# Performance work log

Measured on AMD Instinct MI355X. Metric: run time of the kernel, lower is better.

## Reference

```python
import jax, jax.numpy as jnp
import numpy as np

DIM = 768
H = 12          # num query heads
KV = 6          # num kv heads
GS = H // KV    # group size = 2
HD = DIM // H   # head dim = 64


def setup_inputs() -> dict:
    key = jax.random.key(0)
    ks = jax.random.split(key, 6)
    B, P = 8, 1024
    s = DIM ** -0.5
    x = jax.random.normal(ks[0], (B, P, DIM), dtype=jnp.float32)
    Wq = jax.random.normal(ks[1], (DIM, DIM), dtype=jnp.float32) * s
    Wk = jax.random.normal(ks[2], (DIM, KV * HD), dtype=jnp.float32) * s
    Wv = jax.random.normal(ks[3], (DIM, KV * HD), dtype=jnp.float32) * s
    Wp = jax.random.normal(ks[4], (DIM, DIM), dtype=jnp.float32) * s
    bp = jnp.zeros((DIM,), dtype=jnp.float32)
    return {"x": x, "Wq": Wq, "Wk": Wk, "Wv": Wv, "Wp": Wp, "bp": bp}


def reference(x, Wq, Wk, Wv, Wp, bp):
    B, P, C = x.shape
    scale = HD ** -0.5
    # projections; consecutive heads i*GS..(i+1)*GS-1 form kv-group i (torch.split dim=1)
    q = (x @ Wq).reshape(B, P, KV, GS, HD).transpose(0, 2, 3, 1, 4) * scale  # [B,KV,GS,P,d]
    k = (x @ Wk).reshape(B, P, KV, HD).transpose(0, 2, 1, 3)                 # [B,KV,P,d]
    v = (x @ Wv).reshape(B, P, KV, HD).transpose(0, 2, 1, 3)                 # [B,KV,P,d]

    scores = jnp.einsum('bghqd,bgkd->bghqk', q, k)      # [B,KV,GS,P,P]
    w = jax.nn.softmax(scores, axis=-1)                  # attn_drop=0 (eval)
    att = jnp.einsum('bghqk,bgkd->bghqd', w, v)          # [B,KV,GS,P,d]

    # per-group row-matched gaussian-ish noise (torch get_gaussian), vectorized over KV groups
    y = P * HD
    flat = att.reshape(B, KV, GS, y)                     # rows = groups within kv-group
    M = jax.random.uniform(jax.random.key(42), (KV, GS, y), dtype=flat.dtype)
    di = jnp.arange(min(GS, y))
    M = M.at[:, di, di].set(0.0)                         # sparse: zero diagonal
    m_mean = M.mean(axis=-1, keepdims=True)
    m_std = jnp.std(M, axis=-1, ddof=1, keepdims=True)   # torch.std is unbiased
    m_std = jnp.where(m_std == 0, jnp.ones_like(m_std), m_std)
    Z = (M - m_mean) / m_std                             # [KV,GS,y], shared across batch
    r_mean = flat.mean(axis=-1, keepdims=True)           # [B,KV,GS,1]
    r_std = jnp.std(flat, axis=-1, ddof=1, keepdims=True)
    flat = flat - (Z[None] * r_std + r_mean)

    att = flat.reshape(B, KV, GS, P, HD).reshape(B, H, P, HD)
    out = att.transpose(0, 2, 1, 3).reshape(B, P, C) @ Wp + bp  # proj_drop=0
    return out
```

## Files before the change

kernel.cpp:

```cpp
#include <hip/hip_runtime.h>
#include <hip/hip_bf16.h>
#include <math.h>


#define NTHREADS 256

typedef __bf16 bf16x8 __attribute__((ext_vector_type(8)));
typedef float f32x4 __attribute__((ext_vector_type(4)));

#define MFMA16(a, b, c) __builtin_amdgcn_mfma_f32_16x16x32_bf16(a, b, c, 0, 0, 0)

#define QSCALE 0.18033688011112042f

__device__ __forceinline__ float fexp2(float x) {
#if __has_builtin(__builtin_amdgcn_exp2f)
    return __builtin_amdgcn_exp2f(x);
#else
    return __expf(x * 0.6931471805599453f);
#endif
}

__device__ __forceinline__ void gload16(const void* g, void* l) {
    __builtin_amdgcn_global_load_lds(
        (const __attribute__((address_space(1))) void*)g,
        (__attribute__((address_space(3))) void*)l, 16, 0, 0);
}

__device__ __forceinline__ unsigned rotl_u32(unsigned x, int r) {
    return (x << r) | (x >> (32 - r));
}
__device__ __forceinline__ void threefry_0_42(unsigned x0, unsigned x1,
                                              unsigned& o0, unsigned& o1) {
    const unsigned ks0 = 0u, ks1 = 42u, ks2 = 0u ^ 42u ^ 0x1BD11BDAu;
    x0 += ks0; x1 += ks1;
#define R4(a,b,c,d) \
    x0 += x1; x1 = rotl_u32(x1,a); x1 ^= x0; \
    x0 += x1; x1 = rotl_u32(x1,b); x1 ^= x0; \
    x0 += x1; x1 = rotl_u32(x1,c); x1 ^= x0; \
    x0 += x1; x1 = rotl_u32(x1,d); x1 ^= x0;
    R4(13,15,26,6)   x0 += ks1; x1 += ks2 + 1u;
    R4(17,29,16,24)  x0 += ks2; x1 += ks0 + 2u;
    R4(13,15,26,6)   x0 += ks0; x1 += ks1 + 3u;
    R4(17,29,16,24)  x0 += ks1; x1 += ks2 + 4u;
    R4(13,15,26,6)   x0 += ks2; x1 += ks0 + 5u;
#undef R4
    o0 = x0; o1 = x1;
}
__device__ __forceinline__ float tf_uniform(unsigned i) {
    unsigned o0, o1;
    threefry_0_42(0u, i, o0, o1);
    unsigned bits = o0 ^ o1;
    return __uint_as_float((bits >> 9) | 0x3f800000u) - 1.0f;
}

__device__ __forceinline__ float wave_sum64(float v) {
#pragma unroll
    for (int off = 32; off; off >>= 1) v += __shfl_xor(v, off, 64);
    return v;
}

__device__ __forceinline__ unsigned short bf16_rne(float x) {
    unsigned u = __float_as_uint(x);
    return (unsigned short)((u + 0x7fffu + ((u >> 16) & 1u)) >> 16);
}
__device__ __forceinline__ unsigned pack_bf16x2(float lo, float hi) {
    return (unsigned)bf16_rne(lo) | ((unsigned)bf16_rne(hi) << 16);
}
__device__ __forceinline__ float bfu(unsigned v) {
    return __uint_as_float(v << 16);
}

__global__ __launch_bounds__(NTHREADS) void prep_k(
    const float* __restrict__ x, const float* __restrict__ Wq,
    const float* __restrict__ Wk, const float* __restrict__ Wv,
    const float* __restrict__ Wp,
    unsigned short* __restrict__ xb, unsigned short* __restrict__ wqt,
    unsigned short* __restrict__ wkt, unsigned short* __restrict__ wvt,
    unsigned short* __restrict__ wpt,
    unsigned short* __restrict__ zb, float* __restrict__ zpart)
{
    __shared__ float rbuf[8];
    int blk = blockIdx.x;
    if (blk < 1536) {
#pragma unroll
        for (int j = 0; j < 4; ++j) {
            int i = blk * 1024 + j * 256 + threadIdx.x;
            float4 v = ((const float4*)x)[i];
            uint2 u;
            u.x = pack_bf16x2(v.x, v.y);
            u.y = pack_bf16x2(v.z, v.w);
            *(uint2*)(xb + (size_t)i * 4) = u;
        }
    } else if (blk < 1920) {
        int zc = blk - 1536;
        int row = zc >> 5, chunk = zc & 31;
        int g = row & 1;
        int j0 = chunk * 2048;
        float sum = 0.f, sumsq = 0.f;
        for (int t = threadIdx.x; t < 2048; t += NTHREADS) {
            int j = j0 + t;
            unsigned i = (unsigned)row * 65536u + (unsigned)j;
            float m = tf_uniform(i);
            if (j == g) m = 0.f;
            zb[i] = bf16_rne(m);
            sum += m; sumsq += m * m;
        }
        sum = wave_sum64(sum); sumsq = wave_sum64(sumsq);
        int lane = threadIdx.x & 63, wv = threadIdx.x >> 6;
        if (lane == 0) { rbuf[wv] = sum; rbuf[4 + wv] = sumsq; }
        __syncthreads();
        if (threadIdx.x == 0) {
            zpart[zc * 2]     = rbuf[0] + rbuf[1] + rbuf[2] + rbuf[3];
            zpart[zc * 2 + 1] = rbuf[4] + rbuf[5] + rbuf[6] + rbuf[7];
        }
    } else {
        int id = blk - 1920;
        const float* W; unsigned short* Wt; int N;
        if (id < 144)      { W = Wq; Wt = wqt; N = 768; }
        else if (id < 216) { W = Wk; Wt = wkt; N = 384; id -= 144; }
        else if (id < 288) { W = Wv; Wt = wvt; N = 384; id -= 216; }
        else               { W = Wp; Wt = wpt; N = 768; id -= 288; }
        int ntn = N >> 6;
        int kt = id / ntn, nt = id % ntn;
        int k0 = kt * 64, n0 = nt * 64;
        int t = threadIdx.x;
        int tn = t & 63, tk = t >> 6;
        float r[16];
#pragma unroll
        for (int j = 0; j < 16; ++j)
            r[j] = W[(size_t)(k0 + tk * 16 + j) * N + n0 + tn];
        uint4 u0, u1;
        u0.x = pack_bf16x2(r[0], r[1]);   u0.y = pack_bf16x2(r[2], r[3]);
        u0.z = pack_bf16x2(r[4], r[5]);   u0.w = pack_bf16x2(r[6], r[7]);
        u1.x = pack_bf16x2(r[8], r[9]);   u1.y = pack_bf16x2(r[10], r[11]);
        u1.z = pack_bf16x2(r[12], r[13]); u1.w = pack_bf16x2(r[14], r[15]);
        unsigned short* dst = Wt + (size_t)(n0 + tn) * 768 + k0 + tk * 16;
        *(uint4*)dst = u0;
        *(uint4*)(dst + 8) = u1;
    }
}

__device__ __forceinline__ void mfma_tile_compute(
    const unsigned short* __restrict__ A, const unsigned short* __restrict__ Bt,
    int row0, int col0,
    unsigned short* As, unsigned short* Bs, f32x4 acc[4][4])
{
    const int tid = threadIdx.x;
    const int w = tid >> 6, lane = tid & 63;
    const int c = lane & 15, g = lane >> 4;
    const int m0 = (w & 1) * 64, n0 = (w >> 1) * 64;

#pragma unroll
    for (int mi = 0; mi < 4; ++mi)
#pragma unroll
        for (int ni = 0; ni < 4; ++ni) acc[mi][ni] = (f32x4){0.f, 0.f, 0.f, 0.f};

    const unsigned short* Ag0 = A + (size_t)(row0 + w * 16 + c) * 768 + g * 8;
    const unsigned short* Ag1 = A + (size_t)(row0 + (w + 4) * 16 + c) * 768 + g * 8;
    const unsigned short* Bg0 = Bt + (size_t)(col0 + w * 16 + c) * 768 + g * 8;
    const unsigned short* Bg1 = Bt + (size_t)(col0 + (w + 4) * 16 + c) * 768 + g * 8;
    unsigned short* Al0 = As + w * 1024 + lane * 8;
    unsigned short* Al1 = As + (w + 4) * 1024 + lane * 8;
    unsigned short* Bl0 = Bs + w * 1024 + lane * 8;
    unsigned short* Bl1 = Bs + (w + 4) * 1024 + lane * 8;

    for (int k0 = 0; k0 < 768; k0 += 64) {
        __syncthreads();
        gload16(Ag0 + k0,      Al0);
        gload16(Ag0 + k0 + 32, Al0 + 512);
        gload16(Ag1 + k0,      Al1);
        gload16(Ag1 + k0 + 32, Al1 + 512);
        gload16(Bg0 + k0,      Bl0);
        gload16(Bg0 + k0 + 32, Bl0 + 512);
        gload16(Bg1 + k0,      Bl1);
        gload16(Bg1 + k0 + 32, Bl1 + 512);
        __syncthreads();
#pragma unroll
        for (int ks = 0; ks < 2; ++ks) {
            bf16x8 aA[4], bB[4];
#pragma unroll
            for (int mi = 0; mi < 4; ++mi)
                aA[mi] = *(const bf16x8*)&As[(size_t)((m0 >> 4) + mi) * 1024 + ks * 512 + g * 128 + c * 8];
#pragma unroll
            for (int ni = 0; ni < 4; ++ni)
                bB[ni] = *(const bf16x8*)&Bs[(size_t)((n0 >> 4) + ni) * 1024 + ks * 512 + g * 128 + c * 8];
#pragma unroll
            for (int mi = 0; mi < 4; ++mi)
#pragma unroll
                for (int ni = 0; ni < 4; ++ni)
                    acc[mi][ni] = MFMA16(aA[mi], bB[ni], acc[mi][ni]);
        }
    }
}

__global__ __launch_bounds__(NTHREADS) void qkv_mfma_k(
    const unsigned short* __restrict__ xb, const unsigned short* __restrict__ wqt,
    const unsigned short* __restrict__ wkt, const unsigned short* __restrict__ wvt,
    unsigned short* __restrict__ qbh, unsigned short* __restrict__ kb2,
    unsigned short* __restrict__ vb2)
{
    __shared__ unsigned short As[8192];
    __shared__ unsigned short Bs[8192];
    int id = blockIdx.x;
    int xcd = id & 7, slot = id >> 3;
    int y0i = xcd + ((slot & 7) << 3);
    int nb  = slot >> 3;
    int y0 = y0i * 128;
    f32x4 acc[4][4];

    const int tid = threadIdx.x;
    const int w = tid >> 6, lane = tid & 63;
    const int c = lane & 15, g = lane >> 4;
    const int m0 = (w & 1) * 64, n0 = (w >> 1) * 64;

    if (nb < 9) {
        int row0 = (nb < 6) ? nb * 128 : (nb - 6) * 128;
        const unsigned short* Wt = (nb < 6) ? wqt : wkt;
        mfma_tile_compute(Wt, xb, row0, y0, As, Bs, acc);
        float scale = (nb < 6) ? QSCALE : 1.0f;
#pragma unroll
        for (int mi = 0; mi < 4; ++mi) {
            int ocol = row0 + m0 + mi * 16 + g * 4;
#pragma unroll
            for (int ni = 0; ni < 4; ++ni) {
                int pglob = y0 + n0 + ni * 16 + c;
                int b = pglob >> 10, pin = pglob & 1023;
                ushort4 u;
                u.x = bf16_rne(acc[mi][ni][0] * scale);
                u.y = bf16_rne(acc[mi][ni][1] * scale);
                u.z = bf16_rne(acc[mi][ni][2] * scale);
                u.w = bf16_rne(acc[mi][ni][3] * scale);
                if (nb < 6) {
                    int h = ocol >> 6, d0 = ocol & 63;
                    *(ushort4*)&qbh[(((size_t)b * 12 + h) * 1024 + pin) * 64 + d0] = u;
                } else {
                    int kv = ocol >> 6, d0 = ocol & 63;
                    int kt = pin >> 7, key = pin & 127;
                    *(ushort4*)&kb2[((((size_t)(b * 6 + kv) * 8 + kt) * 8 + (d0 >> 3)) * 128
                                     + key) * 8 + (d0 & 7)] = u;
                }
            }
        }
    } else {
        int col0 = (nb - 9) * 128;
        mfma_tile_compute(xb, wvt, y0, col0, As, Bs, acc);
#pragma unroll
        for (int mi = 0; mi < 4; ++mi) {
            int pglob = y0 + m0 + mi * 16 + g * 4;
            int b = pglob >> 10, pin = pglob & 1023;
            int kt = pin >> 7, pg = (pin & 127) >> 3, p8 = pin & 7;
#pragma unroll
            for (int ni = 0; ni < 4; ++ni) {
                int vcol = col0 + n0 + ni * 16 + c;
                int kv = vcol >> 6, d = vcol & 63;
                ushort4 u;
                u.x = bf16_rne(acc[mi][ni][0]);
                u.y = bf16_rne(acc[mi][ni][1]);
                u.z = bf16_rne(acc[mi][ni][2]);
                u.w = bf16_rne(acc[mi][ni][3]);
                *(ushort4*)&vb2[((((size_t)(b * 6 + kv) * 8 + kt) * 16 + pg) * 64 + d) * 8 + p8] = u;
            }
        }
    }
}

__global__ __launch_bounds__(NTHREADS) void proj_mfma_k(
    const unsigned short* __restrict__ attb, const unsigned short* __restrict__ wpt,
    const float* __restrict__ bp, float* __restrict__ out)
{
    __shared__ unsigned short As[8192];
    __shared__ unsigned short Bs[8192];
    int id = blockIdx.x;
    int xcd = id & 7, slot = id >> 3;
    int col0i = xcd + ((slot & 7) << 3);
    int row0i = slot >> 3;
    int row0 = row0i * 128, col0 = col0i * 128;
    f32x4 acc[4][4];
    mfma_tile_compute(wpt, attb, row0, col0, As, Bs, acc);

    const int tid = threadIdx.x;
    const int w = tid >> 6, lane = tid & 63;
    const int c = lane & 15, g = lane >> 4;
    const int m0 = (w & 1) * 64, n0 = (w >> 1) * 64;
#pragma unroll
    for (int mi = 0; mi < 4; ++mi) {
        int ocol = row0 + m0 + mi * 16 + g * 4;
        float4 bias = *(const float4*)&bp[ocol];
#pragma unroll
        for (int ni = 0; ni < 4; ++ni) {
            int p = col0 + n0 + ni * 16 + c;
            float4 u;
            u.x = acc[mi][ni][0] + bias.x;
            u.y = acc[mi][ni][1] + bias.y;
            u.z = acc[mi][ni][2] + bias.z;
            u.w = acc[mi][ni][3] + bias.w;
            *(float4*)&out[(size_t)p * 768 + ocol] = u;
        }
    }
}

#define LDP 136
__global__ __launch_bounds__(NTHREADS) void attn_mfma_k(
    const unsigned short* __restrict__ qbh, const unsigned short* __restrict__ kb2,
    const unsigned short* __restrict__ vb2, unsigned short* __restrict__ attb,
    float* __restrict__ spart)
{
    __shared__ unsigned short P_lds[4 * 32 * LDP];
    __shared__ float l_s[4][32];
    __shared__ float sbuf[8];

    int id = blockIdx.x;
    int xcd = id & 7, slot = id >> 3;
    int grp = slot % 6, member = slot / 6;
    int g48 = xcd + 8 * grp;
    int b = g48 / 6, kv = g48 % 6;
    int h = kv * 2 + (member & 1);
    int qtile = member >> 1;
    const int qt0 = qtile * 128;

    const int tid = threadIdx.x;
    const int w = tid >> 6, lane = tid & 63;
    const int c = lane & 15, g = lane >> 4;

    const unsigned short* qh = qbh + (((size_t)b * 12 + h) * 1024 + qt0 + w * 32) * 64;
    const unsigned short* kbase = kb2 + ((size_t)(b * 6 + kv) * 8) * 8192;
    const unsigned short* vbase = vb2 + ((size_t)(b * 6 + kv) * 8) * 8192;
    unsigned short* Pw = P_lds + w * 32 * LDP;

    bf16x8 bQ[2][2];
#pragma unroll
    for (int ks = 0; ks < 2; ++ks) {
        bQ[ks][0] = *(const bf16x8*)(qh + (size_t)(c) * 64 + ks * 32 + g * 8);
        bQ[ks][1] = *(const bf16x8*)(qh + (size_t)(16 + c) * 64 + ks * 32 + g * 8);
    }

    f32x4 O[2][4];
#pragma unroll
    for (int i = 0; i < 2; ++i)
#pragma unroll
        for (int j = 0; j < 4; ++j) O[i][j] = (f32x4){0.f, 0.f, 0.f, 0.f};
    float l_r[2] = {0.f, 0.f};

    for (int t = 0; t < 8; ++t) {
        const unsigned short* kt = kbase + (size_t)t * 8192;
        const unsigned short* vt = vbase + (size_t)t * 8192;

        bf16x8 aK[2][8];
#pragma unroll
        for (int ks = 0; ks < 2; ++ks)
#pragma unroll
            for (int mb = 0; mb < 8; ++mb)
                aK[ks][mb] = *(const bf16x8*)(kt + ((size_t)(ks * 4 + g) * 128 + mb * 16 + c) * 8);

        f32x4 S[8][2];
#pragma unroll
        for (int mb = 0; mb < 8; ++mb) {
            S[mb][0] = (f32x4){0.f, 0.f, 0.f, 0.f};
            S[mb][1] = (f32x4){0.f, 0.f, 0.f, 0.f};
        }
#pragma unroll
        for (int ks = 0; ks < 2; ++ks)
#pragma unroll
            for (int mb = 0; mb < 8; ++mb) {
                S[mb][0] = MFMA16(aK[ks][mb], bQ[ks][0], S[mb][0]);
                S[mb][1] = MFMA16(aK[ks][mb], bQ[ks][1], S[mb][1]);
            }

        bf16x8 bV[4][4];
#pragma unroll
        for (int ks = 0; ks < 4; ++ks)
#pragma unroll
            for (int nb = 0; nb < 4; ++nb)
                bV[ks][nb] = *(const bf16x8*)(vt + ((size_t)(ks * 4 + g) * 64 + nb * 16 + c) * 8);

#pragma unroll
        for (int qn = 0; qn < 2; ++qn) {
            float lt = 0.f;
#pragma unroll
            for (int mb = 0; mb < 8; ++mb) {
                float p0 = fexp2(S[mb][qn][0]);
                float p1 = fexp2(S[mb][qn][1]);
                float p2 = fexp2(S[mb][qn][2]);
                float p3 = fexp2(S[mb][qn][3]);
                lt += (p0 + p1) + (p2 + p3);
                uint2 uu;
                uu.x = pack_bf16x2(p0, p1);
                uu.y = pack_bf16x2(p2, p3);
                *(uint2*)&Pw[(size_t)(qn * 16 + c) * LDP + mb * 16 + g * 4] = uu;
            }
            lt += __shfl_xor(lt, 16, 64);
            lt += __shfl_xor(lt, 32, 64);
            l_r[qn] += lt;
        }

#pragma unroll
        for (int ks = 0; ks < 4; ++ks) {
            bf16x8 aP0 = *(const bf16x8*)&Pw[(size_t)(c) * LDP + ks * 32 + g * 8];
            bf16x8 aP1 = *(const bf16x8*)&Pw[(size_t)(16 + c) * LDP + ks * 32 + g * 8];
#pragma unroll
            for (int nb = 0; nb < 4; ++nb) {
                O[0][nb] = MFMA16(aP0, bV[ks][nb], O[0][nb]);
                O[1][nb] = MFMA16(aP1, bV[ks][nb], O[1][nb]);
            }
        }
    }
    if (g == 0) { l_s[w][c] = l_r[0]; l_s[w][16 + c] = l_r[1]; }
    f32x4 li0 = *(f32x4*)&l_s[w][g * 4];
    f32x4 li1 = *(f32x4*)&l_s[w][16 + g * 4];
    float inv0[4], inv1[4];
#pragma unroll
    for (int r = 0; r < 4; ++r) { inv0[r] = 1.f / li0[r]; inv1[r] = 1.f / li1[r]; }
    unsigned short* ob = attb + ((size_t)b * 1024 + qt0 + w * 32) * 768 + h * 64;
    float psum = 0.f, psumsq = 0.f;
#pragma unroll
    for (int r = 0; r < 4; ++r) {
#pragma unroll
        for (int nb = 0; nb < 4; ++nb) {
            float o0 = O[0][nb][r] * inv0[r];
            float o1 = O[1][nb][r] * inv1[r];
            psum += o0 + o1;
            psumsq += o0 * o0 + o1 * o1;
            ob[(size_t)(g * 4 + r) * 768 + nb * 16 + c]      = bf16_rne(o0);
            ob[(size_t)(16 + g * 4 + r) * 768 + nb * 16 + c] = bf16_rne(o1);
        }
    }
    psum = wave_sum64(psum); psumsq = wave_sum64(psumsq);
    if (lane == 0) { sbuf[w] = psum; sbuf[4 + w] = psumsq; }
    __syncthreads();
    if (tid == 0) {
        int idx = ((b * 12 + h) * 8 + qtile) * 2;
        spart[idx]     = sbuf[0] + sbuf[1] + sbuf[2] + sbuf[3];
        spart[idx + 1] = sbuf[4] + sbuf[5] + sbuf[6] + sbuf[7];
    }
}

__global__ __launch_bounds__(NTHREADS) void stats2_k(
    unsigned short* __restrict__ attb, const unsigned short* __restrict__ zb,
    const float* __restrict__ spart, const float* __restrict__ zpart)
{
    int blk = blockIdx.x;
    int bh = blk >> 3, ch = blk & 7;
    int b = bh / 12, h = bh % 12;
    float zs = 0.f, zs2 = 0.f, rs = 0.f, rs2 = 0.f;
#pragma unroll
    for (int cc = 0; cc < 32; ++cc) {
        zs  += zpart[(h * 32 + cc) * 2];
        zs2 += zpart[(h * 32 + cc) * 2 + 1];
    }
#pragma unroll
    for (int cc = 0; cc < 8; ++cc) {
        rs  += spart[(bh * 8 + cc) * 2];
        rs2 += spart[(bh * 8 + cc) * 2 + 1];
    }
    float m_mean = zs * (1.f / 65536.f);
    float m_var  = (zs2 - 65536.f * m_mean * m_mean) * (1.f / 65535.f);
    float m_sd   = sqrtf(fmaxf(m_var, 0.f));
    if (m_sd == 0.f) m_sd = 1.f;
    float r_mean = rs * (1.f / 65536.f);
    float r_var  = (rs2 - 65536.f * r_mean * r_mean) * (1.f / 65535.f);
    float r_sd   = sqrtf(fmaxf(r_var, 0.f));
    float a = r_sd / m_sd;
    float bc = m_mean * a - r_mean;

    unsigned short* base = attb + ((size_t)b * 1024 + ch * 128) * 768 + h * 64;
    const unsigned short* zrow = zb + (size_t)h * 65536 + (size_t)ch * 8192;
    for (int f = threadIdx.x; f < 1024; f += NTHREADS) {
        int p = f >> 3, dq = (f & 7) * 8;
        unsigned short* ptr = base + (size_t)p * 768 + dq;
        uint4 u = *(const uint4*)ptr;
        uint4 zu = *(const uint4*)(zrow + (size_t)f * 8);
        float v0 = bfu(u.x)       - bfu(zu.x)       * a + bc;
        float v1 = bfu(u.x >> 16) - bfu(zu.x >> 16) * a + bc;
        float v2 = bfu(u.y)       - bfu(zu.y)       * a + bc;
        float v3 = bfu(u.y >> 16) - bfu(zu.y >> 16) * a + bc;
        float v4 = bfu(u.z)       - bfu(zu.z)       * a + bc;
        float v5 = bfu(u.z >> 16) - bfu(zu.z >> 16) * a + bc;
        float v6 = bfu(u.w)       - bfu(zu.w)       * a + bc;
        float v7 = bfu(u.w >> 16) - bfu(zu.w >> 16) * a + bc;
        uint4 o;
        o.x = pack_bf16x2(v0, v1);
        o.y = pack_bf16x2(v2, v3);
        o.z = pack_bf16x2(v4, v5);
        o.w = pack_bf16x2(v6, v7);
        *(uint4*)ptr = o;
    }
}

extern "C" void kernel_launch(void* const* d_in, const int* in_sizes, int n_in,
                              void* d_out, int out_size, void* d_ws, size_t ws_size,
                              hipStream_t stream) {
    const float* x  = (const float*)d_in[0];
    const float* Wq = (const float*)d_in[1];
    const float* Wk = (const float*)d_in[2];
    const float* Wv = (const float*)d_in[3];
    const float* Wp = (const float*)d_in[4];
    const float* bp = (const float*)d_in[5];
    float* out = (float*)d_out;

    float* ws    = (float*)d_ws;
    float* zpart = ws;
    float* spart = zpart + 768;
    unsigned short* zb   = (unsigned short*)(spart + 1536);
    unsigned short* xb   = zb + 786432;
    unsigned short* wqt  = xb + 6291456;
    unsigned short* wkt  = wqt + 589824;
    unsigned short* wvt  = wkt + 294912;
    unsigned short* wpt  = wvt + 294912;
    unsigned short* qbh  = wpt + 589824;
    unsigned short* kb2  = qbh + 6291456;
    unsigned short* vb2  = kb2 + 3145728;
    unsigned short* attb = vb2 + 3145728;

    prep_k<<<2352, NTHREADS, 0, stream>>>(x, Wq, Wk, Wv, Wp,
                                          xb, wqt, wkt, wvt, wpt, zb, zpart);
    qkv_mfma_k<<<768, NTHREADS, 0, stream>>>(xb, wqt, wkt, wvt, qbh, kb2, vb2);
    attn_mfma_k<<<768, NTHREADS, 0, stream>>>(qbh, kb2, vb2, attb, spart);
    stats2_k<<<768, NTHREADS, 0, stream>>>(attb, zb, spart, zpart);
    proj_mfma_k<<<384, NTHREADS, 0, stream>>>(attb, wpt, bp, out);
}
```

Before: 218.1 us.

## Shrink GEMM tiles to 64x128 to double block count for QKV and projection

Replaces the 128x128 MFMA tile routine with a 64x128 variant: each of four waves computes 64x32 outputs, and the six global-to-LDS segments per thread are split across A and B. The QKV and projection launches double their grids (1536 and 768 blocks) with remapped block indexing, so the 256 CUs see more waves and less tail imbalance. The cost is lower arithmetic intensity per tile, since each loaded B tile is reused across fewer A rows, giving more redundant global traffic.

```diff
diff --git a/kernel.cpp b/kernel.cpp
--- a/kernel.cpp
+++ b/kernel.cpp
@@ -140,54 +140,53 @@
     }
 }
 
-__device__ __forceinline__ void mfma_tile_compute(
+__device__ __forceinline__ void mfma_tile64(
     const unsigned short* __restrict__ A, const unsigned short* __restrict__ Bt,
     int row0, int col0,
-    unsigned short* As, unsigned short* Bs, f32x4 acc[4][4])
+    unsigned short* As, unsigned short* Bs, f32x4 acc[4][2])
 {
     const int tid = threadIdx.x;
     const int w = tid >> 6, lane = tid & 63;
     const int c = lane & 15, g = lane >> 4;
-    const int m0 = (w & 1) * 64, n0 = (w >> 1) * 64;
 
 #pragma unroll
     for (int mi = 0; mi < 4; ++mi)
 #pragma unroll
-        for (int ni = 0; ni < 4; ++ni) acc[mi][ni] = (f32x4){0.f, 0.f, 0.f, 0.f};
-
-    const unsigned short* Ag0 = A + (size_t)(row0 + w * 16 + c) * 768 + g * 8;
-    const unsigned short* Ag1 = A + (size_t)(row0 + (w + 4) * 16 + c) * 768 + g * 8;
-    const unsigned short* Bg0 = Bt + (size_t)(col0 + w * 16 + c) * 768 + g * 8;
-    const unsigned short* Bg1 = Bt + (size_t)(col0 + (w + 4) * 16 + c) * 768 + g * 8;
-    unsigned short* Al0 = As + w * 1024 + lane * 8;
-    unsigned short* Al1 = As + (w + 4) * 1024 + lane * 8;
-    unsigned short* Bl0 = Bs + w * 1024 + lane * 8;
-    unsigned short* Bl1 = Bs + (w + 4) * 1024 + lane * 8;
+        for (int ni = 0; ni < 2; ++ni) acc[mi][ni] = (f32x4){0.f, 0.f, 0.f, 0.f};
+
+    const unsigned short* gsrc[6];
+    unsigned short* ldst[6];
+#pragma unroll
+    for (int j = 0; j < 6; ++j) {
+        int seg = w * 6 + j;
+        bool isA = seg < 8;
+        int s = isA ? seg : seg - 8;
+        int chunk = s >> 1, kh = s & 1;
+        const unsigned short* gb = isA
+            ? (A  + (size_t)(row0 + chunk * 16 + c) * 768)
+            : (Bt + (size_t)(col0 + chunk * 16 + c) * 768);
+        gsrc[j] = gb + kh * 32 + g * 8;
+        ldst[j] = (isA ? As : Bs) + chunk * 1024 + kh * 512 + lane * 8;
+    }
 
     for (int k0 = 0; k0 < 768; k0 += 64) {
         __syncthreads();
-        gload16(Ag0 + k0,      Al0);
-        gload16(Ag0 + k0 + 32, Al0 + 512);
-        gload16(Ag1 + k0,      Al1);
-        gload16(Ag1 + k0 + 32, Al1 + 512);
-        gload16(Bg0 + k0,      Bl0);
-        gload16(Bg0 + k0 + 32, Bl0 + 512);
-        gload16(Bg1 + k0,      Bl1);
-        gload16(Bg1 + k0 + 32, Bl1 + 512);
+#pragma unroll
+        for (int j = 0; j < 6; ++j) gload16(gsrc[j] + k0, ldst[j]);
         __syncthreads();
 #pragma unroll
         for (int ks = 0; ks < 2; ++ks) {
-            bf16x8 aA[4], bB[4];
+            bf16x8 aA[4], bB[2];
 #pragma unroll
             for (int mi = 0; mi < 4; ++mi)
-                aA[mi] = *(const bf16x8*)&As[(size_t)((m0 >> 4) + mi) * 1024 + ks * 512 + g * 128 + c * 8];
-#pragma unroll
-            for (int ni = 0; ni < 4; ++ni)
-                bB[ni] = *(const bf16x8*)&Bs[(size_t)((n0 >> 4) + ni) * 1024 + ks * 512 + g * 128 + c * 8];
+                aA[mi] = *(const bf16x8*)&As[mi * 1024 + ks * 512 + g * 128 + c * 8];
+#pragma unroll
+            for (int ni = 0; ni < 2; ++ni)
+                bB[ni] = *(const bf16x8*)&Bs[(w * 2 + ni) * 1024 + ks * 512 + g * 128 + c * 8];
 #pragma unroll
             for (int mi = 0; mi < 4; ++mi)
 #pragma unroll
-                for (int ni = 0; ni < 4; ++ni)
+                for (int ni = 0; ni < 2; ++ni)
                     acc[mi][ni] = MFMA16(aA[mi], bB[ni], acc[mi][ni]);
         }
     }
@@ -199,38 +198,38 @@
     unsigned short* __restrict__ qbh, unsigned short* __restrict__ kb2,
     unsigned short* __restrict__ vb2)
 {
-    __shared__ unsigned short As[8192];
+    __shared__ unsigned short As[4096];
     __shared__ unsigned short Bs[8192];
     int id = blockIdx.x;
     int xcd = id & 7, slot = id >> 3;
-    int y0i = xcd + ((slot & 7) << 3);
-    int nb  = slot >> 3;
-    int y0 = y0i * 128;
-    f32x4 acc[4][4];
+    f32x4 acc[4][2];
 
     const int tid = threadIdx.x;
     const int w = tid >> 6, lane = tid & 63;
     const int c = lane & 15, g = lane >> 4;
-    const int m0 = (w & 1) * 64, n0 = (w >> 1) * 64;
-
-    if (nb < 9) {
-        int row0 = (nb < 6) ? nb * 128 : (nb - 6) * 128;
-        const unsigned short* Wt = (nb < 6) ? wqt : wkt;
-        mfma_tile_compute(Wt, xb, row0, y0, As, Bs, acc);
-        float scale = (nb < 6) ? QSCALE : 1.0f;
+
+    if (slot < 144) {
+        int y0i = xcd + ((slot & 7) << 3);
+        int nb = slot >> 3;
+        int y0 = y0i * 128;
+        bool isq = nb < 12;
+        int row0 = isq ? nb * 64 : (nb - 12) * 64;
+        const unsigned short* Wt = isq ? wqt : wkt;
+        mfma_tile64(Wt, xb, row0, y0, As, Bs, acc);
+        float scale = isq ? QSCALE : 1.0f;
 #pragma unroll
         for (int mi = 0; mi < 4; ++mi) {
-            int ocol = row0 + m0 + mi * 16 + g * 4;
-#pragma unroll
-            for (int ni = 0; ni < 4; ++ni) {
-                int pglob = y0 + n0 + ni * 16 + c;
+            int ocol = row0 + mi * 16 + g * 4;
+#pragma unroll
+            for (int ni = 0; ni < 2; ++ni) {
+                int pglob = y0 + w * 32 + ni * 16 + c;
                 int b = pglob >> 10, pin = pglob & 1023;
                 ushort4 u;
                 u.x = bf16_rne(acc[mi][ni][0] * scale);
                 u.y = bf16_rne(acc[mi][ni][1] * scale);
                 u.z = bf16_rne(acc[mi][ni][2] * scale);
                 u.w = bf16_rne(acc[mi][ni][3] * scale);
-                if (nb < 6) {
+                if (isq) {
                     int h = ocol >> 6, d0 = ocol & 63;
                     *(ushort4*)&qbh[(((size_t)b * 12 + h) * 1024 + pin) * 64 + d0] = u;
                 } else {
@@ -242,16 +241,19 @@
             }
         }
     } else {
-        int col0 = (nb - 9) * 128;
-        mfma_tile_compute(xb, wvt, y0, col0, As, Bs, acc);
+        int s = slot - 144;
+        int ct = s >> 4;
+        int pt = xcd + ((s & 15) << 3);
+        int row0 = pt * 64, col0 = ct * 128;
+        mfma_tile64(xb, wvt, row0, col0, As, Bs, acc);
 #pragma unroll
         for (int mi = 0; mi < 4; ++mi) {
-            int pglob = y0 + m0 + mi * 16 + g * 4;
+            int pglob = row0 + mi * 16 + g * 4;
             int b = pglob >> 10, pin = pglob & 1023;
             int kt = pin >> 7, pg = (pin & 127) >> 3, p8 = pin & 7;
 #pragma unroll
-            for (int ni = 0; ni < 4; ++ni) {
-                int vcol = col0 + n0 + ni * 16 + c;
+            for (int ni = 0; ni < 2; ++ni) {
+                int vcol = col0 + w * 32 + ni * 16 + c;
                 int kv = vcol >> 6, d = vcol & 63;
                 ushort4 u;
                 u.x = bf16_rne(acc[mi][ni][0]);
@@ -268,27 +270,26 @@
     const unsigned short* __restrict__ attb, const unsigned short* __restrict__ wpt,
     const float* __restrict__ bp, float* __restrict__ out)
 {
-    __shared__ unsigned short As[8192];
+    __shared__ unsigned short As[4096];
     __shared__ unsigned short Bs[8192];
     int id = blockIdx.x;
     int xcd = id & 7, slot = id >> 3;
     int col0i = xcd + ((slot & 7) << 3);
     int row0i = slot >> 3;
-    int row0 = row0i * 128, col0 = col0i * 128;
-    f32x4 acc[4][4];
-    mfma_tile_compute(wpt, attb, row0, col0, As, Bs, acc);
+    int row0 = row0i * 64, col0 = col0i * 128;
+    f32x4 acc[4][2];
+    mfma_tile64(wpt, attb, row0, col0, As, Bs, acc);
 
     const int tid = threadIdx.x;
     const int w = tid >> 6, lane = tid & 63;
     const int c = lane & 15, g = lane >> 4;
-    const int m0 = (w & 1) * 64, n0 = (w >> 1) * 64;
 #pragma unroll
     for (int mi = 0; mi < 4; ++mi) {
-        int ocol = row0 + m0 + mi * 16 + g * 4;
+        int ocol = row0 + mi * 16 + g * 4;
         float4 bias = *(const float4*)&bp[ocol];
 #pragma unroll
-        for (int ni = 0; ni < 4; ++ni) {
-            int p = col0 + n0 + ni * 16 + c;
+        for (int ni = 0; ni < 2; ++ni) {
+            int p = col0 + w * 32 + ni * 16 + c;
             float4 u;
             u.x = acc[mi][ni][0] + bias.x;
             u.y = acc[mi][ni][1] + bias.y;
@@ -513,8 +514,8 @@
 
     prep_k<<<2352, NTHREADS, 0, stream>>>(x, Wq, Wk, Wv, Wp,
                                           xb, wqt, wkt, wvt, wpt, zb, zpart);
-    qkv_mfma_k<<<768, NTHREADS, 0, stream>>>(xb, wqt, wkt, wvt, qbh, kb2, vb2);
+    qkv_mfma_k<<<1536, NTHREADS, 0, stream>>>(xb, wqt, wkt, wvt, qbh, kb2, vb2);
     attn_mfma_k<<<768, NTHREADS, 0, stream>>>(qbh, kb2, vb2, attb, spart);
     stats2_k<<<768, NTHREADS, 0, stream>>>(attb, zb, spart, zpart);
-    proj_mfma_k<<<384, NTHREADS, 0, stream>>>(attb, wpt, bp, out);
-}
+    proj_mfma_k<<<768, NTHREADS, 0, stream>>>(attb, wpt, bp, out);
+}
```

Result: slower. 230.0 us (+5.5%).
